# Kernel tuning notes

Measured on AMD Instinct MI355X. Metric: run time of the kernel, lower is better.

## Reference

```python
import jax, jax.numpy as jnp
import numpy as np

DIM = 1024
NUM_HEADS = 16
HEAD_DIM = DIM // NUM_HEADS
SCALE = HEAD_DIM ** -0.5


def setup_inputs() -> dict:
    key = jax.random.key(0)
    ks = jax.random.split(key, 5)
    x = jax.random.normal(ks[0], (4, 1024, DIM), dtype=jnp.float32)
    w_qkv = jax.random.normal(ks[1], (DIM, 3 * DIM), dtype=jnp.float32) * (DIM ** -0.5)
    b_qkv = jnp.zeros((3 * DIM,), dtype=jnp.float32)
    w_proj = jax.random.normal(ks[2], (DIM, DIM), dtype=jnp.float32) * (DIM ** -0.5)
    b_proj = jnp.zeros((DIM,), dtype=jnp.float32)
    return {"x": x, "w_qkv": w_qkv, "b_qkv": b_qkv, "w_proj": w_proj, "b_proj": b_proj}


def reference(x, w_qkv, b_qkv, w_proj, b_proj):
    B, N, C = x.shape
    qkv = x @ w_qkv + b_qkv                                  # [B, N, 3C]
    qkv = qkv.reshape(B, N, 3, NUM_HEADS, HEAD_DIM)
    qkv = jnp.transpose(qkv, (2, 0, 3, 1, 4))                # [3, B, H, N, d]
    q, k, v = qkv[0] * SCALE, qkv[1], qkv[2]
    # attn scores in float32 (clamp to finfo range is a no-op after the cast)
    attn = jnp.einsum('bhnd,bhmd->bhnm', q, k).astype(jnp.float32)
    f32 = jnp.finfo(jnp.float32)
    attn = jnp.clip(attn, f32.min, f32.max)
    attn = jax.nn.softmax(attn, axis=-1)
    out = jnp.einsum('bhnm,bhmd->bhnd', attn, v)             # [B, H, N, d]
    out = jnp.transpose(out, (0, 2, 1, 3)).reshape(B, N, C)
    return out @ w_proj + b_proj
```

## Files before the change

kernel.cpp:

```cpp
#include <hip/hip_runtime.h>


typedef _Float16 half8 __attribute__((ext_vector_type(8)));
typedef _Float16 half4v __attribute__((ext_vector_type(4)));
typedef float floatx4 __attribute__((ext_vector_type(4)));

#define MFMA16(a, b, c) __builtin_amdgcn_mfma_f32_16x16x32_f16((a), (b), (c), 0, 0, 0)

static constexpr int DIM = 1024;
static constexpr int BATCH = 4;
static constexpr int SEQ = 1024;
static constexpr int NH = 16;
static constexpr int HD = 64;
static constexpr float SCALE = 0.125f;

__device__ static inline void gld16(_Float16* lds, const _Float16* g) {
    __builtin_amdgcn_global_load_lds(
        (const __attribute__((address_space(1))) void*)g,
        (__attribute__((address_space(3))) void*)lds, 16, 0, 0);
}

__global__ __launch_bounds__(256) void prep(const float* __restrict__ x,
                                            _Float16* __restrict__ xh,
                                            const float* __restrict__ wqkv,
                                            _Float16* __restrict__ wqkvT,
                                            const float* __restrict__ wproj,
                                            _Float16* __restrict__ wprojT) {
    __shared__ float tile[32][33];
    const int bid = blockIdx.x;
    const int tid = threadIdx.x;
    if (bid < 4096) {
        int i = (bid * 256 + tid) * 4;
        float4 v = *reinterpret_cast<const float4*>(x + i);
        half4v h;
        h[0] = (_Float16)v.x; h[1] = (_Float16)v.y;
        h[2] = (_Float16)v.z; h[3] = (_Float16)v.w;
        *reinterpret_cast<half4v*>(xh + i) = h;
        return;
    }
    const float* in;
    _Float16* out;
    int R, C, bx, by;
    if (bid < 7168) {
        int b = bid - 4096;
        in = wqkv; out = wqkvT; R = 1024; C = 3072;
        bx = b % 96; by = b / 96;
    } else {
        int b = bid - 7168;
        in = wproj; out = wprojT; R = 1024; C = 1024;
        bx = b & 31; by = b >> 5;
    }
    const int c0 = bx * 32, r0 = by * 32;
    const int tx = tid & 31, ty = tid >> 5;
#pragma unroll
    for (int j = 0; j < 32; j += 8)
        tile[ty + j][tx] = in[(size_t)(r0 + ty + j) * C + (c0 + tx)];
    __syncthreads();
#pragma unroll
    for (int j = 0; j < 32; j += 8)
        out[(size_t)(c0 + ty + j) * R + (r0 + tx)] = (_Float16)tile[tx][ty + j];
}

template <int MODE>
__global__ __launch_bounds__(256, 2) void gemm_bt(const _Float16* __restrict__ A,
                                                  const _Float16* __restrict__ Bt,
                                                  const float* __restrict__ bias, int N,
                                                  float* __restrict__ outF,
                                                  _Float16* __restrict__ qbuf,
                                                  _Float16* __restrict__ kbuf,
                                                  _Float16* __restrict__ vtbuf) {
    constexpr int K = 1024;
    constexpr int BK = 32;
    __shared__ _Float16 Ah[2][128 * BK];
    __shared__ _Float16 Bh[2][128 * BK];

    const int tid = threadIdx.x;
    const int wid = tid >> 6;
    const int lane = tid & 63;
    const int g = lane >> 4;
    const int ln = lane & 15;
    const int wr = wid >> 1, wc = wid & 1;
    const int m0 = blockIdx.y * 128;
    const int n0 = blockIdx.x * 128;

    floatx4 acc[4][4];
#pragma unroll
    for (int i = 0; i < 4; ++i)
#pragma unroll
        for (int j = 0; j < 4; ++j) acc[i][j] = (floatx4){0.f, 0.f, 0.f, 0.f};

    const int lrow = lane >> 2;
    const int lk = (lane & 3) * 8;
    const _Float16* ga0 = A + (size_t)(m0 + wid * 16 + lrow) * K + lk;
    const _Float16* gb0 = Bt + (size_t)(n0 + wid * 16 + lrow) * K + lk;

    gld16(&Ah[0][(wid * 16) * BK], ga0);
    gld16(&Ah[0][(64 + wid * 16) * BK], ga0 + (size_t)64 * K);
    gld16(&Bh[0][(wid * 16) * BK], gb0);
    gld16(&Bh[0][(64 + wid * 16) * BK], gb0 + (size_t)64 * K);

    for (int kt = 0; kt < K / BK; ++kt) {
        const int cur = kt & 1;
        asm volatile("s_waitcnt vmcnt(0)" ::: "memory");
        asm volatile("s_barrier" ::: "memory");
        if (kt < K / BK - 1) {
            const int k0 = (kt + 1) * BK;
            gld16(&Ah[cur ^ 1][(wid * 16) * BK], ga0 + k0);
            gld16(&Ah[cur ^ 1][(64 + wid * 16) * BK], ga0 + (size_t)64 * K + k0);
            gld16(&Bh[cur ^ 1][(wid * 16) * BK], gb0 + k0);
            gld16(&Bh[cur ^ 1][(64 + wid * 16) * BK], gb0 + (size_t)64 * K + k0);
        }

        half8 af[4], bf[4];
#pragma unroll
        for (int i = 0; i < 4; ++i)
            af[i] = *reinterpret_cast<const half8*>(
                &Ah[cur][(wr * 64 + i * 16 + ln) * BK + g * 8]);
#pragma unroll
        for (int j = 0; j < 4; ++j)
            bf[j] = *reinterpret_cast<const half8*>(
                &Bh[cur][(wc * 64 + j * 16 + ln) * BK + g * 8]);
#pragma unroll
        for (int i = 0; i < 4; ++i)
#pragma unroll
            for (int j = 0; j < 4; ++j) acc[i][j] = MFMA16(af[i], bf[j], acc[i][j]);
    }

#pragma unroll
    for (int i = 0; i < 4; ++i) {
#pragma unroll
        for (int j = 0; j < 4; ++j) {
            const int n = n0 + wc * 64 + j * 16 + ln;
            const float bn = bias[n];
            const int mrow = m0 + wr * 64 + i * 16 + g * 4;
            if (MODE == 0) {
                const int which = n >> 10;
                const int rem = n & 1023;
                const int h = rem >> 6;
                const int dd = rem & 63;
                const int b = mrow >> 10, tok = mrow & 1023;
                const int bh = b * NH + h;
                if (which == 2) {
                    half4v pk;
#pragma unroll
                    for (int r = 0; r < 4; ++r) pk[r] = (_Float16)(acc[i][j][r] + bn);
                    *reinterpret_cast<half4v*>(
                        &vtbuf[(size_t)((bh * HD + dd) << 10) + tok]) = pk;
                } else {
                    _Float16* dst = (which == 0) ? qbuf : kbuf;
                    const float sc = (which == 0) ? SCALE : 1.0f;
#pragma unroll
                    for (int r = 0; r < 4; ++r)
                        dst[(size_t)((bh << 10) + tok + r) * HD + dd] =
                            (_Float16)((acc[i][j][r] + bn) * sc);
                }
            } else {
#pragma unroll
                for (int r = 0; r < 4; ++r)
                    outF[(size_t)(mrow + r) * N + n] = acc[i][j][r] + bn;
            }
        }
    }
}

__global__ __launch_bounds__(256, 2) void flash_attn(const _Float16* __restrict__ qbuf,
                                                     const _Float16* __restrict__ kbuf,
                                                     const _Float16* __restrict__ vtbuf,
                                                     _Float16* __restrict__ attn_out) {
    __shared__ _Float16 Klds[2 * 2 * 64 * 32];
    __shared__ _Float16 Vlds[2 * 2 * 64 * 32];
    __shared__ _Float16 Plds[8 * 16 * 68];

    const int tid = threadIdx.x;
    const int wid = tid >> 6;
    const int lane = tid & 63;
    const int g = lane >> 4;
    const int ln = lane & 15;
    const int bh = blockIdx.x;
    const int qbase = blockIdx.y * 128 + wid * 32;
    const _Float16* qg = qbuf + ((size_t)bh << 10) * HD;
    const _Float16* kg = kbuf + ((size_t)bh << 10) * HD;
    const _Float16* vg = vtbuf + (size_t)bh * (HD * SEQ);

    const int srow = lane >> 2;
    const int sch = (lane & 3) * 8;

    half8 qf[2][2];
#pragma unroll
    for (int rg = 0; rg < 2; ++rg)
#pragma unroll
        for (int f = 0; f < 2; ++f)
            qf[rg][f] = *reinterpret_cast<const half8*>(
                qg + (size_t)(qbase + rg * 16 + ln) * HD + f * 32 + g * 8);

    floatx4 o[2][4];
#pragma unroll
    for (int rg = 0; rg < 2; ++rg)
#pragma unroll
        for (int t = 0; t < 4; ++t) o[rg][t] = (floatx4){0.f, 0.f, 0.f, 0.f};
    float l_lane[2][4] = {{0.f, 0.f, 0.f, 0.f}, {0.f, 0.f, 0.f, 0.f}};

    _Float16* Pw = Plds + (wid * 2) * 16 * 68;

#pragma unroll
    for (int f = 0; f < 2; ++f) {
        gld16(Klds + f * 2048 + (wid * 16) * 32,
              kg + (size_t)(wid * 16 + srow) * HD + f * 32 + sch);
        gld16(Vlds + f * 2048 + (wid * 16) * 32,
              vg + (size_t)(wid * 16 + srow) * SEQ + f * 32 + sch);
    }

    for (int kt = 0; kt < SEQ / 64; ++kt) {
        asm volatile("s_waitcnt vmcnt(0)" ::: "memory");
        asm volatile("s_barrier" ::: "memory");
        const int cur = kt & 1;
        if (kt < SEQ / 64 - 1) {
            const int kr1 = (kt + 1) * 64;
            _Float16* kb = Klds + (cur ^ 1) * 4096;
            _Float16* vb = Vlds + (cur ^ 1) * 4096;
#pragma unroll
            for (int f = 0; f < 2; ++f) {
                gld16(kb + f * 2048 + (wid * 16) * 32,
                      kg + (size_t)(kr1 + wid * 16 + srow) * HD + f * 32 + sch);
                gld16(vb + f * 2048 + (wid * 16) * 32,
                      vg + (size_t)(wid * 16 + srow) * SEQ + kr1 + f * 32 + sch);
            }
        }
        const _Float16* Kb = Klds + cur * 4096;
        const _Float16* Vb = Vlds + cur * 4096;

        half8 kf[4][2], vf[4][2];
#pragma unroll
        for (int c = 0; c < 4; ++c)
#pragma unroll
            for (int f = 0; f < 2; ++f) {
                kf[c][f] = *reinterpret_cast<const half8*>(
                    &Kb[f * 2048 + (c * 16 + ln) * 32 + g * 8]);
                vf[c][f] = *reinterpret_cast<const half8*>(
                    &Vb[f * 2048 + (c * 16 + ln) * 32 + g * 8]);
            }

        floatx4 s[2][4];
#pragma unroll
        for (int rg = 0; rg < 2; ++rg)
#pragma unroll
            for (int c = 0; c < 4; ++c) {
                floatx4 z = (floatx4){0.f, 0.f, 0.f, 0.f};
                z = MFMA16(qf[rg][0], kf[c][0], z);
                z = MFMA16(qf[rg][1], kf[c][1], z);
                s[rg][c] = z;
            }

#pragma unroll
        for (int rg = 0; rg < 2; ++rg)
#pragma unroll
            for (int c = 0; c < 4; ++c)
#pragma unroll
                for (int r = 0; r < 4; ++r) {
                    float p = __expf(s[rg][c][r]);
                    l_lane[rg][r] += p;
                    Pw[(rg * 16 + g * 4 + r) * 68 + c * 16 + ln] = (_Float16)p;
                }

        asm volatile("s_waitcnt lgkmcnt(0)" ::: "memory");

#pragma unroll
        for (int rg = 0; rg < 2; ++rg) {
            half8 pf0 = *reinterpret_cast<const half8*>(&Pw[(rg * 16 + ln) * 68 + g * 8]);
            half8 pf1 = *reinterpret_cast<const half8*>(&Pw[(rg * 16 + ln) * 68 + 32 + g * 8]);
#pragma unroll
            for (int t = 0; t < 4; ++t) {
                o[rg][t] = MFMA16(pf0, vf[t][0], o[rg][t]);
                o[rg][t] = MFMA16(pf1, vf[t][1], o[rg][t]);
            }
        }
    }

    const int b = bh >> 4, h = bh & 15;
#pragma unroll
    for (int rg = 0; rg < 2; ++rg)
#pragma unroll
        for (int r = 0; r < 4; ++r) {
            float l = l_lane[rg][r];
            l += __shfl_xor(l, 1);
            l += __shfl_xor(l, 2);
            l += __shfl_xor(l, 4);
            l += __shfl_xor(l, 8);
            const float inv = 1.0f / l;
            const int tok = qbase + rg * 16 + g * 4 + r;
            _Float16* dst = attn_out + (size_t)(b * SEQ + tok) * DIM + h * HD;
#pragma unroll
            for (int t = 0; t < 4; ++t) dst[t * 16 + ln] = (_Float16)(o[rg][t][r] * inv);
        }
}

extern "C" void kernel_launch(void* const* d_in, const int* in_sizes, int n_in,
                              void* d_out, int out_size, void* d_ws, size_t ws_size,
                              hipStream_t stream) {
    const float* x = (const float*)d_in[0];
    const float* wqkv = (const float*)d_in[1];
    const float* bqkv = (const float*)d_in[2];
    const float* wproj = (const float*)d_in[3];
    const float* bproj = (const float*)d_in[4];
    float* out = (float*)d_out;

    char* ws = (char*)d_ws;
    _Float16* xh     = (_Float16*)(ws);
    _Float16* wqkvT  = (_Float16*)(ws + (8ull << 20));
    _Float16* qbuf   = (_Float16*)(ws + (14ull << 20));
    _Float16* kbuf   = (_Float16*)(ws + (22ull << 20));
    _Float16* vtbuf  = (_Float16*)(ws + (30ull << 20));
    _Float16* wprojT = (_Float16*)(ws + (38ull << 20));
    _Float16* attn   = xh;

    prep<<<8192, 256, 0, stream>>>(x, xh, wqkv, wqkvT, wproj, wprojT);
    gemm_bt<0><<<dim3(24, 32), 256, 0, stream>>>(xh, wqkvT, bqkv, 3 * DIM, nullptr,
                                                 qbuf, kbuf, vtbuf);
    flash_attn<<<dim3(BATCH * NH, SEQ / 128), 256, 0, stream>>>(qbuf, kbuf, vtbuf, attn);
    gemm_bt<1><<<dim3(8, 32), 256, 0, stream>>>(attn, wprojT, bproj, DIM, out,
                                                nullptr, nullptr, nullptr);
}
```

Baseline: 184.1 us.

## Pre-tile operands into K-panel layout and triple-buffer GEMM and attention loads

Intermediate fp16 buffers (x, transposed weights, K, V^T, attention output) are now stored in 32-wide K-panel blocks. Each wave's global_load_lds then reads one contiguous 1 KB chunk instead of strided rows. The GEMM and flash-attention loops move from double to triple buffering with a prefetch distance of two and vmcnt(4) waits, so loads overlap more compute. In exchange, LDS use per block goes up and every producer and consumer index must agree on the new layout.

```diff
diff --git a/kernel.cpp b/kernel.cpp
--- a/kernel.cpp
+++ b/kernel.cpp
@@ -35,19 +35,21 @@
         half4v h;
         h[0] = (_Float16)v.x; h[1] = (_Float16)v.y;
         h[2] = (_Float16)v.z; h[3] = (_Float16)v.w;
-        *reinterpret_cast<half4v*>(xh + i) = h;
+        const int m = i >> 10, k = i & 1023;
+        *reinterpret_cast<half4v*>(
+            &xh[((size_t)(k >> 5) * 4096 + m) * 32 + (k & 31)]) = h;
         return;
     }
     const float* in;
     _Float16* out;
-    int R, C, bx, by;
+    int C, NN, bx, by;
     if (bid < 7168) {
         int b = bid - 4096;
-        in = wqkv; out = wqkvT; R = 1024; C = 3072;
+        in = wqkv; out = wqkvT; C = 3072; NN = 3072;
         bx = b % 96; by = b / 96;
     } else {
         int b = bid - 7168;
-        in = wproj; out = wprojT; R = 1024; C = 1024;
+        in = wproj; out = wprojT; C = 1024; NN = 1024;
         bx = b & 31; by = b >> 5;
     }
     const int c0 = bx * 32, r0 = by * 32;
@@ -58,7 +60,8 @@
     __syncthreads();
 #pragma unroll
     for (int j = 0; j < 32; j += 8)
-        out[(size_t)(c0 + ty + j) * R + (r0 + tx)] = (_Float16)tile[tx][ty + j];
+        out[((size_t)(r0 >> 5) * NN + (c0 + ty + j)) * 32 + tx] =
+            (_Float16)tile[tx][ty + j];
 }
 
 template <int MODE>
@@ -69,10 +72,9 @@
                                                   _Float16* __restrict__ qbuf,
                                                   _Float16* __restrict__ kbuf,
                                                   _Float16* __restrict__ vtbuf) {
-    constexpr int K = 1024;
-    constexpr int BK = 32;
-    __shared__ _Float16 Ah[2][128 * BK];
-    __shared__ _Float16 Bh[2][128 * BK];
+    constexpr int NT = 32;
+    __shared__ _Float16 Ah[3 * 4096];
+    __shared__ _Float16 Bh[3 * 4096];
 
     const int tid = threadIdx.x;
     const int wid = tid >> 6;
@@ -82,6 +84,12 @@
     const int wr = wid >> 1, wc = wid & 1;
     const int m0 = blockIdx.y * 128;
     const int n0 = blockIdx.x * 128;
+    const size_t PA = (size_t)4096 * 32;
+    const size_t PB = (size_t)N * 32;
+    const int woff = wid * 1024;
+    const int l8 = lane * 8;
+    const _Float16* ga = A + (size_t)m0 * 32 + woff + l8;
+    const _Float16* gb = Bt + (size_t)n0 * 32 + woff + l8;
 
     floatx4 acc[4][4];
 #pragma unroll
@@ -89,37 +97,37 @@
 #pragma unroll
         for (int j = 0; j < 4; ++j) acc[i][j] = (floatx4){0.f, 0.f, 0.f, 0.f};
 
-    const int lrow = lane >> 2;
-    const int lk = (lane & 3) * 8;
-    const _Float16* ga0 = A + (size_t)(m0 + wid * 16 + lrow) * K + lk;
-    const _Float16* gb0 = Bt + (size_t)(n0 + wid * 16 + lrow) * K + lk;
-
-    gld16(&Ah[0][(wid * 16) * BK], ga0);
-    gld16(&Ah[0][(64 + wid * 16) * BK], ga0 + (size_t)64 * K);
-    gld16(&Bh[0][(wid * 16) * BK], gb0);
-    gld16(&Bh[0][(64 + wid * 16) * BK], gb0 + (size_t)64 * K);
-
-    for (int kt = 0; kt < K / BK; ++kt) {
-        const int cur = kt & 1;
-        asm volatile("s_waitcnt vmcnt(0)" ::: "memory");
+#pragma unroll
+    for (int t = 0; t < 2; ++t) {
+        gld16(&Ah[t * 4096 + woff], ga + t * PA);
+        gld16(&Ah[t * 4096 + woff + 512], ga + t * PA + 512);
+        gld16(&Bh[t * 4096 + woff], gb + t * PB);
+        gld16(&Bh[t * 4096 + woff + 512], gb + t * PB + 512);
+    }
+
+    for (int kt = 0; kt < NT; ++kt) {
+        if (kt < NT - 1) asm volatile("s_waitcnt vmcnt(4)" ::: "memory");
+        else             asm volatile("s_waitcnt vmcnt(0)" ::: "memory");
         asm volatile("s_barrier" ::: "memory");
-        if (kt < K / BK - 1) {
-            const int k0 = (kt + 1) * BK;
-            gld16(&Ah[cur ^ 1][(wid * 16) * BK], ga0 + k0);
-            gld16(&Ah[cur ^ 1][(64 + wid * 16) * BK], ga0 + (size_t)64 * K + k0);
-            gld16(&Bh[cur ^ 1][(wid * 16) * BK], gb0 + k0);
-            gld16(&Bh[cur ^ 1][(64 + wid * 16) * BK], gb0 + (size_t)64 * K + k0);
-        }
+        if (kt < NT - 2) {
+            const int pf = (kt + 2) % 3;
+            const size_t ka = (size_t)(kt + 2) * PA;
+            const size_t kb = (size_t)(kt + 2) * PB;
+            gld16(&Ah[pf * 4096 + woff], ga + ka);
+            gld16(&Ah[pf * 4096 + woff + 512], ga + ka + 512);
+            gld16(&Bh[pf * 4096 + woff], gb + kb);
+            gld16(&Bh[pf * 4096 + woff + 512], gb + kb + 512);
+        }
+        const _Float16* Ac = &Ah[(kt % 3) * 4096];
+        const _Float16* Bc = &Bh[(kt % 3) * 4096];
 
         half8 af[4], bf[4];
 #pragma unroll
         for (int i = 0; i < 4; ++i)
-            af[i] = *reinterpret_cast<const half8*>(
-                &Ah[cur][(wr * 64 + i * 16 + ln) * BK + g * 8]);
+            af[i] = *reinterpret_cast<const half8*>(&Ac[(wr * 64 + i * 16 + ln) * 32 + g * 8]);
 #pragma unroll
         for (int j = 0; j < 4; ++j)
-            bf[j] = *reinterpret_cast<const half8*>(
-                &Bh[cur][(wc * 64 + j * 16 + ln) * BK + g * 8]);
+            bf[j] = *reinterpret_cast<const half8*>(&Bc[(wc * 64 + j * 16 + ln) * 32 + g * 8]);
 #pragma unroll
         for (int i = 0; i < 4; ++i)
 #pragma unroll
@@ -145,14 +153,18 @@
 #pragma unroll
                     for (int r = 0; r < 4; ++r) pk[r] = (_Float16)(acc[i][j][r] + bn);
                     *reinterpret_cast<half4v*>(
-                        &vtbuf[(size_t)((bh * HD + dd) << 10) + tok]) = pk;
+                        &vtbuf[((size_t)(bh * 32 + (tok >> 5)) * 64 + dd) * 32 +
+                               (tok & 31)]) = pk;
+                } else if (which == 1) {
+#pragma unroll
+                    for (int r = 0; r < 4; ++r)
+                        kbuf[((size_t)(bh * 2 + (dd >> 5)) * SEQ + tok + r) * 32 +
+                             (dd & 31)] = (_Float16)(acc[i][j][r] + bn);
                 } else {
-                    _Float16* dst = (which == 0) ? qbuf : kbuf;
-                    const float sc = (which == 0) ? SCALE : 1.0f;
 #pragma unroll
                     for (int r = 0; r < 4; ++r)
-                        dst[(size_t)((bh << 10) + tok + r) * HD + dd] =
-                            (_Float16)((acc[i][j][r] + bn) * sc);
+                        qbuf[(size_t)((bh << 10) + tok + r) * HD + dd] =
+                            (_Float16)((acc[i][j][r] + bn) * SCALE);
                 }
             } else {
 #pragma unroll
@@ -167,8 +179,8 @@
                                                      const _Float16* __restrict__ kbuf,
                                                      const _Float16* __restrict__ vtbuf,
                                                      _Float16* __restrict__ attn_out) {
-    __shared__ _Float16 Klds[2 * 2 * 64 * 32];
-    __shared__ _Float16 Vlds[2 * 2 * 64 * 32];
+    __shared__ _Float16 Klds[3 * 4096];
+    __shared__ _Float16 Vlds[3 * 4096];
     __shared__ _Float16 Plds[8 * 16 * 68];
 
     const int tid = threadIdx.x;
@@ -179,11 +191,11 @@
     const int bh = blockIdx.x;
     const int qbase = blockIdx.y * 128 + wid * 32;
     const _Float16* qg = qbuf + ((size_t)bh << 10) * HD;
-    const _Float16* kg = kbuf + ((size_t)bh << 10) * HD;
-    const _Float16* vg = vtbuf + (size_t)bh * (HD * SEQ);
-
-    const int srow = lane >> 2;
-    const int sch = (lane & 3) * 8;
+    const _Float16* kg = kbuf + (size_t)bh * (2 * SEQ * 32);
+    const _Float16* vg = vtbuf + (size_t)bh * (32 * 64 * 32);
+
+    const int woff = wid * 512;
+    const int l8 = lane * 8;
 
     half8 qf[2][2];
 #pragma unroll
@@ -200,34 +212,37 @@
         for (int t = 0; t < 4; ++t) o[rg][t] = (floatx4){0.f, 0.f, 0.f, 0.f};
     float l_lane[2][4] = {{0.f, 0.f, 0.f, 0.f}, {0.f, 0.f, 0.f, 0.f}};
 
-    _Float16* Pw = Plds + (wid * 2) * 16 * 68;
-
-#pragma unroll
-    for (int f = 0; f < 2; ++f) {
-        gld16(Klds + f * 2048 + (wid * 16) * 32,
-              kg + (size_t)(wid * 16 + srow) * HD + f * 32 + sch);
-        gld16(Vlds + f * 2048 + (wid * 16) * 32,
-              vg + (size_t)(wid * 16 + srow) * SEQ + f * 32 + sch);
-    }
-
-    for (int kt = 0; kt < SEQ / 64; ++kt) {
-        asm volatile("s_waitcnt vmcnt(0)" ::: "memory");
+    _Float16* Pw = Plds + wid * (2 * 16 * 68);
+
+    constexpr int NT = SEQ / 64;
+#pragma unroll
+    for (int t = 0; t < 2; ++t) {
+#pragma unroll
+        for (int f = 0; f < 2; ++f) {
+            gld16(&Klds[t * 4096 + f * 2048 + woff],
+                  kg + (size_t)f * (SEQ * 32) + t * 64 * 32 + woff + l8);
+            gld16(&Vlds[t * 4096 + f * 2048 + woff],
+                  vg + (size_t)(2 * t + f) * 2048 + woff + l8);
+        }
+    }
+
+    for (int kt = 0; kt < NT; ++kt) {
+        if (kt < NT - 1) asm volatile("s_waitcnt vmcnt(4)" ::: "memory");
+        else             asm volatile("s_waitcnt vmcnt(0)" ::: "memory");
         asm volatile("s_barrier" ::: "memory");
-        const int cur = kt & 1;
-        if (kt < SEQ / 64 - 1) {
-            const int kr1 = (kt + 1) * 64;
-            _Float16* kb = Klds + (cur ^ 1) * 4096;
-            _Float16* vb = Vlds + (cur ^ 1) * 4096;
+        if (kt < NT - 2) {
+            const int pf = (kt + 2) % 3;
+            const int krp = (kt + 2) * 64;
 #pragma unroll
             for (int f = 0; f < 2; ++f) {
-                gld16(kb + f * 2048 + (wid * 16) * 32,
-                      kg + (size_t)(kr1 + wid * 16 + srow) * HD + f * 32 + sch);
-                gld16(vb + f * 2048 + (wid * 16) * 32,
-                      vg + (size_t)(wid * 16 + srow) * SEQ + kr1 + f * 32 + sch);
-            }
-        }
-        const _Float16* Kb = Klds + cur * 4096;
-        const _Float16* Vb = Vlds + cur * 4096;
+                gld16(&Klds[pf * 4096 + f * 2048 + woff],
+                      kg + (size_t)f * (SEQ * 32) + krp * 32 + woff + l8);
+                gld16(&Vlds[pf * 4096 + f * 2048 + woff],
+                      vg + (size_t)(2 * (kt + 2) + f) * 2048 + woff + l8);
+            }
+        }
+        const _Float16* Kb = &Klds[(kt % 3) * 4096];
+        const _Float16* Vb = &Vlds[(kt % 3) * 4096];
 
         half8 kf[4][2], vf[4][2];
 #pragma unroll
@@ -288,9 +303,10 @@
             l += __shfl_xor(l, 8);
             const float inv = 1.0f / l;
             const int tok = qbase + rg * 16 + g * 4 + r;
-            _Float16* dst = attn_out + (size_t)(b * SEQ + tok) * DIM + h * HD;
-#pragma unroll
-            for (int t = 0; t < 4; ++t) dst[t * 16 + ln] = (_Float16)(o[rg][t][r] * inv);
+#pragma unroll
+            for (int t = 0; t < 4; ++t)
+                attn_out[((size_t)(h * 2 + (t >> 1)) * 4096 + (b * SEQ + tok)) * 32 +
+                         (t & 1) * 16 + ln] = (_Float16)(o[rg][t][r] * inv);
         }
 }
 
```

Result: no change. 183.4 us (-0.4%).
